# Optimization experiments

Measured on AMD Instinct MI355X. Metric: run time of the kernel, lower is better.

## Reference

```python
import jax, jax.numpy as jnp
import numpy as np

K = 20
EPS = 1e-5


def knn_idx(x, k):
    # x: (B, N, C) -> (B, N, k) indices of k nearest neighbors (incl. self)
    xx = jnp.sum(x * x, axis=-1, keepdims=True)           # (B,N,1)
    inner = -2.0 * jnp.einsum('bnc,bmc->bnm', x, x)        # (B,N,N)
    pd = -xx - inner - jnp.swapaxes(xx, 1, 2)              # negative sq dist
    _, idx = jax.lax.top_k(pd, k)                          # (B,N,k)
    return idx


def get_graph_feature(x, k=K):
    B, N, C = x.shape
    idx = knn_idx(x, k)                                    # (B,N,k)
    # gather neighbor features per batch
    feature = jax.vmap(lambda xb, ib: xb[ib])(x, idx)      # (B,N,k,C)
    xe = jnp.broadcast_to(x[:, :, None, :], (B, N, k, C))  # (B,N,k,C)
    f = jnp.concatenate([feature - xe, xe], axis=3)        # (B,N,k,2C)
    return jnp.transpose(f, (0, 3, 1, 2))                  # (B,2C,N,k)


def conv1x1(x, W, b):
    # x: (B,Cin,N,k), W: (Cout,Cin)
    return jnp.einsum('bcnk,oc->bonk', x, W) + b[None, :, None, None]


def batchnorm(x, gamma, beta):
    # training-mode BN over (B,N,k) per channel, biased variance (torch default)
    mean = jnp.mean(x, axis=(0, 2, 3), keepdims=True)
    var = jnp.var(x, axis=(0, 2, 3), keepdims=True)
    xhat = (x - mean) * jax.lax.rsqrt(var + EPS)
    return xhat * gamma[None, :, None, None] + beta[None, :, None, None]


def setup_inputs() -> dict:
    key = jax.random.key(0)
    ks = jax.random.split(key, 10)
    B, N, C = 4, 4096, 3
    x = jax.random.normal(ks[0], (B, N, C), dtype=jnp.float32)
    W1 = jax.random.normal(ks[1], (64, 2 * C), dtype=jnp.float32) * 0.1
    b1 = jnp.zeros((64,), jnp.float32)
    g1 = jnp.ones((64,), jnp.float32)
    be1 = jnp.zeros((64,), jnp.float32)
    W2 = jax.random.normal(ks[2], (128, 64), dtype=jnp.float32) * 0.1
    b2 = jnp.zeros((128,), jnp.float32)
    g2 = jnp.ones((128,), jnp.float32)
    be2 = jnp.zeros((128,), jnp.float32)
    W3 = jax.random.normal(ks[3], (128, 128), dtype=jnp.float32) * 0.1
    b3 = jnp.zeros((128,), jnp.float32)
    g3 = jnp.ones((128,), jnp.float32)
    be3 = jnp.zeros((128,), jnp.float32)
    return {"x": x, "W1": W1, "b1": b1, "g1": g1, "be1": be1,
            "W2": W2, "b2": b2, "g2": g2, "be2": be2,
            "W3": W3, "b3": b3, "g3": g3, "be3": be3}


def reference(x, W1, b1, g1, be1, W2, b2, g2, be2, W3, b3, g3, be3):
    f = get_graph_feature(x, K)                  # (B,6,N,k)
    h = jax.nn.relu(batchnorm(conv1x1(f, W1, b1), g1, be1))
    h = jax.nn.relu(batchnorm(conv1x1(h, W2, b2), g2, be2))
    h = batchnorm(conv1x1(h, W3, b3), g3, be3)
    return jnp.max(h, axis=-1)                   # (B,128,N)
```

## Files before the change

### kernel.cpp

```cpp
#include <hip/hip_runtime.h>


typedef __attribute__((ext_vector_type(8)))  short short8;
typedef __attribute__((ext_vector_type(4)))  float floatx4;

#define BATCH 4
#define NPTS  4096
#define KNN   20
#define BN_   (BATCH*NPTS)
#define CNT   (BATCH*NPTS*KNN)

__device__ __forceinline__ unsigned short f2bf(float f) {
  unsigned u = __float_as_uint(f);
  unsigned r = u + 0x7FFFu + ((u >> 16) & 1u);
  return (unsigned short)(r >> 16);
}

__device__ __forceinline__ short8 pack8(float a, float b, float c, float d,
                                        float e, float f, float g, float h) {
  short8 r;
  r[0]=(short)f2bf(a); r[1]=(short)f2bf(b); r[2]=(short)f2bf(c); r[3]=(short)f2bf(d);
  r[4]=(short)f2bf(e); r[5]=(short)f2bf(f); r[6]=(short)f2bf(g); r[7]=(short)f2bf(h);
  return r;
}

__device__ __forceinline__ unsigned mono(float f) {
  unsigned u = __float_as_uint(f);
  return u ^ ((unsigned)((int)u >> 31) | 0x80000000u);
}

__global__ void pf_prep(const float* __restrict__ x, float4* __restrict__ xp,
                        float* __restrict__ stats) {
  int pt = blockIdx.x * 256 + threadIdx.x;
  float x0 = x[pt*3+0], x1 = x[pt*3+1], x2 = x[pt*3+2];
  float xx = x0*x0 + x1*x1 + x2*x2;
  xp[pt] = make_float4(x0, x1, x2, xx);
  if (blockIdx.x == 0)
    for (int i = threadIdx.x; i < 640; i += 256) stats[i] = 0.0f;
}

__device__ __forceinline__ float sort_take20th(float v, int lane) {
  #pragma unroll
  for (int k = 2; k <= 64; k <<= 1) {
    #pragma unroll
    for (int j = k >> 1; j >= 1; j >>= 1) {
      float o = __shfl_xor(v, j);
      bool keepmax = (((lane & j) == 0) == ((lane & k) == 0));
      v = keepmax ? fmaxf(v, o) : fminf(v, o);
    }
  }
  return __shfl(v, 19);
}

__device__ __forceinline__ unsigned long long sort64_desc(unsigned long long v,
                                                          int lane) {
  #pragma unroll
  for (int k = 2; k <= 64; k <<= 1) {
    #pragma unroll
    for (int j = k >> 1; j >= 1; j >>= 1) {
      unsigned long long o = __shfl_xor(v, j);
      bool keepmax = (((lane & j) == 0) == ((lane & k) == 0));
      unsigned long long hi = v > o ? v : o;
      unsigned long long lo = v > o ? o : v;
      v = keepmax ? hi : lo;
    }
  }
  return v;
}

__global__ __launch_bounds__(256) void pf_knn(const float4* __restrict__ xp,
                                              int* __restrict__ idxb) {
  __shared__ unsigned long long lst[8][128];
  __shared__ int lcnt[8];
  const int tid  = threadIdx.x;
  const int lane = tid & 63;
  const int w    = tid >> 6;
  const int b    = blockIdx.x >> 9;
  const int nb   = (blockIdx.x & 511) * 8 + w * 2;
  const float4* xb = xp + b * NPTS;

  float4 q0 = xb[nb], q1 = xb[nb + 1];

  float mx0 = -3.0e38f, mx1 = -3.0e38f;
  for (int j0 = 0; j0 < NPTS; j0 += 64) {
    float4 c = xb[j0 + lane];
    float d0 = fmaf(q0.x,c.x, fmaf(q0.y,c.y, q0.z*c.z));
    float d1 = fmaf(q1.x,c.x, fmaf(q1.y,c.y, q1.z*c.z));
    mx0 = fmaxf(mx0, fmaf(2.f,d0,-q0.w) - c.w);
    mx1 = fmaxf(mx1, fmaf(2.f,d1,-q1.w) - c.w);
  }
  float T0 = sort_take20th(mx0, lane);
  float T1 = sort_take20th(mx1, lane);

  if (lane < 2) lcnt[w*2 + lane] = 0;
  __syncthreads();

  for (int j0 = 0; j0 < NPTS; j0 += 64) {
    float4 c = xb[j0 + lane];
    float d0 = fmaf(q0.x,c.x, fmaf(q0.y,c.y, q0.z*c.z));
    float d1 = fmaf(q1.x,c.x, fmaf(q1.y,c.y, q1.z*c.z));
    float p0 = fmaf(2.f,d0,-q0.w) - c.w;
    float p1 = fmaf(2.f,d1,-q1.w) - c.w;
    unsigned long long keybase = (unsigned long long)(4095 - (j0 + lane));
    if (p0 >= T0) {
      int o = atomicAdd(&lcnt[w*2+0], 1);
      if (o < 128) lst[w*2+0][o] = ((unsigned long long)mono(p0) << 32) | keybase;
    }
    if (p1 >= T1) {
      int o = atomicAdd(&lcnt[w*2+1], 1);
      if (o < 128) lst[w*2+1][o] = ((unsigned long long)mono(p1) << 32) | keybase;
    }
  }

  #pragma unroll 1
  for (int i = 0; i < 2; ++i) {
    const int li = w*2 + i;
    const int cn = lcnt[li];
    const int outbase = (b * NPTS + nb + i) * KNN;
    if (cn <= 64) {
      unsigned long long v = (lane < cn) ? lst[li][lane] : 0ull;
      v = sort64_desc(v, lane);
      if (lane < KNN) idxb[outbase + lane] = 4095 - (int)(v & 0xFFFFFFFFull);
    } else if (cn <= 128) {
      unsigned long long e0 = lst[li][lane];
      unsigned long long e1 = (lane + 64 < cn) ? lst[li][lane + 64] : 0ull;
      #pragma unroll 1
      for (int r = 0; r < KNN; ++r) {
        unsigned long long m = e0 > e1 ? e0 : e1;
        #pragma unroll
        for (int o = 32; o; o >>= 1) {
          unsigned long long t = __shfl_xor(m, o);
          m = t > m ? t : m;
        }
        if (lane == 0) idxb[outbase + r] = 4095 - (int)(m & 0xFFFFFFFFull);
        if (e0 == m) e0 = 0ull; else if (e1 == m) e1 = 0ull;
      }
    } else {
      const float4 qq = (i == 0) ? q0 : q1;
      unsigned long long prev = ~0ull;
      #pragma unroll 1
      for (int r = 0; r < KNN; ++r) {
        unsigned long long best = 0ull;
        for (int j0 = 0; j0 < NPTS; j0 += 64) {
          float4 c = xb[j0 + lane];
          float dd = fmaf(qq.x,c.x, fmaf(qq.y,c.y, qq.z*c.z));
          float pd = fmaf(2.f,dd,-qq.w) - c.w;
          unsigned long long key = ((unsigned long long)mono(pd) << 32) |
                                   (unsigned long long)(4095 - (j0 + lane));
          if (key < prev && key > best) best = key;
        }
        #pragma unroll
        for (int o = 32; o; o >>= 1) {
          unsigned long long t = __shfl_xor(best, o);
          best = t > best ? t : best;
        }
        if (lane == 0) idxb[outbase + r] = 4095 - (int)(best & 0xFFFFFFFFull);
        prev = best;
      }
    }
  }
}

__global__ __launch_bounds__(256) void pf_stats1(
    const float4* __restrict__ xp, const int* __restrict__ idxb,
    const float* __restrict__ W1, const float* __restrict__ b1,
    float* __restrict__ gs1, float* __restrict__ gq1) {
  __shared__ float S[64], Q[64];
  const int tid = threadIdx.x;
  const int c = tid & 63, slice = tid >> 6;
  if (tid < 64) { S[tid] = 0.f; Q[tid] = 0.f; }
  __syncthreads();
  const float wa0=W1[c*6+0], wa1=W1[c*6+1], wa2=W1[c*6+2];
  const float wb0=W1[c*6+3], wb1=W1[c*6+4], wb2=W1[c*6+5];
  const float bb = b1[c];
  float s = 0.f, q = 0.f;
  int ptbase = (blockIdx.x * 4 + slice) * 4;
  for (int u = 0; u < 4; ++u) {
    int pt = ptbase + u;
    float4 xi = xp[pt];
    int ib = (pt >> 12) << 12;
    for (int kk = 0; kk < KNN; ++kk) {
      int j = idxb[pt*KNN + kk];
      float4 xj = xp[ib + j];
      float y = bb;
      y = fmaf(wa0, xj.x - xi.x, y);
      y = fmaf(wa1, xj.y - xi.y, y);
      y = fmaf(wa2, xj.z - xi.z, y);
      y = fmaf(wb0, xi.x, y);
      y = fmaf(wb1, xi.y, y);
      y = fmaf(wb2, xi.z, y);
      s += y; q = fmaf(y, y, q);
    }
  }
  atomicAdd(&S[c], s); atomicAdd(&Q[c], q);
  __syncthreads();
  if (tid < 64) { atomicAdd(&gs1[tid], S[tid]); atomicAdd(&gq1[tid], Q[tid]); }
}

__global__ void pf_affine(const float* __restrict__ gs, const float* __restrict__ gq,
                          const float* __restrict__ gamma, const float* __restrict__ beta,
                          const float* __restrict__ bconv, int foldb, int C,
                          float* __restrict__ sc, float* __restrict__ sh) {
  int c = threadIdx.x;
  if (c < C) {
    const float inv = 1.0f / (float)CNT;
    float mean = gs[c] * inv;
    float var  = gq[c] * inv - mean * mean;
    float s = gamma[c] * rsqrtf(var + 1e-5f);
    float shift = beta[c] - mean * s;
    if (foldb) shift = fmaf(s, bconv[c], shift);
    sc[c] = s; sh[c] = shift;
  }
}

__global__ __launch_bounds__(256, 2) void pf_stats2(
    const float4* __restrict__ xp, const int* __restrict__ idxb,
    const float* __restrict__ W1, const float* __restrict__ sc1e,
    const float* __restrict__ sh1e, const float* __restrict__ W2,
    const float* __restrict__ b2,
    float* __restrict__ gs2, float* __restrict__ gq2) {
  __shared__ __align__(16) float4 XI[32];
  __shared__ __align__(16) float4 XJ[32];
  __shared__ __align__(16) unsigned short H1[32][72];
  __shared__ float SS[128], SQ[128];

  const int tid = threadIdx.x;
  const int lane = tid & 63, w = tid >> 6;
  const int chalf = w & 1, rh = w >> 1;
  const int l15 = lane & 15, quad = lane >> 4;
  const int pt0 = blockIdx.x * 32;

  if (tid < 128) { SS[tid] = 0.f; SQ[tid] = 0.f; }
  if (tid < 32)  XI[tid] = xp[pt0 + tid];

  short8 w1f[2];
  #pragma unroll
  for (int t = 0; t < 2; ++t) {
    short8 f = {0,0,0,0,0,0,0,0};
    if (quad == 0) {
      const float* p = W1 + (32*chalf + 16*t + l15) * 6;
      f = pack8(p[0],p[1],p[2],p[3],p[4],p[5],0.f,0.f);
    }
    w1f[t] = f;
  }
  float a1[2], s1[2];
  #pragma unroll
  for (int t = 0; t < 2; ++t) {
    int c = 32*chalf + 16*t + l15;
    a1[t] = sc1e[c]; s1[t] = sh1e[c];
  }
  short8 w2f[2][4];
  #pragma unroll
  for (int ks = 0; ks < 2; ++ks)
    #pragma unroll
    for (int t = 0; t < 4; ++t) {
      const float* p = W2 + (64*chalf + 16*t + l15) * 64 + 32*ks + quad*8;
      w2f[ks][t] = pack8(p[0],p[1],p[2],p[3],p[4],p[5],p[6],p[7]);
    }
  float bb2[4];
  #pragma unroll
  for (int t = 0; t < 4; ++t) bb2[t] = b2[64*chalf + 16*t + l15];

  float sum[4] = {0,0,0,0}, sq[4] = {0,0,0,0};

  for (int kk = 0; kk < KNN; ++kk) {
    if (tid < 32) {
      int pt = pt0 + tid;
      XJ[tid] = xp[((pt >> 12) << 12) + idxb[pt*KNN + kk]];
    }
    __syncthreads();
    short8 af = {0,0,0,0,0,0,0,0};
    if (quad == 0) {
      float4 xi = XI[rh*16 + l15];
      float4 xj = XJ[rh*16 + l15];
      af = pack8(xj.x-xi.x, xj.y-xi.y, xj.z-xi.z, xi.x, xi.y, xi.z, 0.f, 0.f);
    }
    floatx4 acc1[2] = {{0,0,0,0},{0,0,0,0}};
    #pragma unroll
    for (int t = 0; t < 2; ++t)
      acc1[t] = __builtin_amdgcn_mfma_f32_16x16x32_bf16(af, w1f[t], acc1[t], 0,0,0);
    #pragma unroll
    for (int t = 0; t < 2; ++t) {
      int c = 32*chalf + 16*t + l15;
      #pragma unroll
      for (int r = 0; r < 4; ++r) {
        float h = fmaxf(fmaf(a1[t], acc1[t][r], s1[t]), 0.f);
        H1[rh*16 + quad*4 + r][c] = f2bf(h);
      }
    }
    __syncthreads();
    floatx4 acc2[4] = {{0,0,0,0},{0,0,0,0},{0,0,0,0},{0,0,0,0}};
    #pragma unroll
    for (int ks = 0; ks < 2; ++ks) {
      short8 a = *(const short8*)&H1[rh*16 + l15][ks*32 + quad*8];
      #pragma unroll
      for (int t = 0; t < 4; ++t)
        acc2[t] = __builtin_amdgcn_mfma_f32_16x16x32_bf16(a, w2f[ks][t], acc2[t], 0,0,0);
    }
    #pragma unroll
    for (int t = 0; t < 4; ++t)
      #pragma unroll
      for (int r = 0; r < 4; ++r) {
        float v = acc2[t][r] + bb2[t];
        sum[t] += v; sq[t] = fmaf(v, v, sq[t]);
      }
  }
  #pragma unroll
  for (int t = 0; t < 4; ++t) {
    float s = sum[t], z = sq[t];
    s += __shfl_xor(s, 16); z += __shfl_xor(z, 16);
    s += __shfl_xor(s, 32); z += __shfl_xor(z, 32);
    if (quad == 0) {
      int c = 64*chalf + 16*t + l15;
      atomicAdd(&SS[c], s); atomicAdd(&SQ[c], z);
    }
  }
  __syncthreads();
  if (tid < 128) { atomicAdd(&gs2[tid], SS[tid]); atomicAdd(&gq2[tid], SQ[tid]); }
}

__global__ __launch_bounds__(256, 2) void pf_main(
    const float4* __restrict__ xp, const int* __restrict__ idxb,
    const float* __restrict__ W1, const float* __restrict__ sc1e,
    const float* __restrict__ sh1e, const float* __restrict__ W2,
    const float* __restrict__ sc2e, const float* __restrict__ shm2,
    const float* __restrict__ W3, const float* __restrict__ b3,
    float* __restrict__ gs3, float* __restrict__ gq3,
    float* __restrict__ maxv) {
  __shared__ __align__(16) float4 XI[32];
  __shared__ __align__(16) float4 XJ[32];
  __shared__ __align__(16) unsigned short H1[32][72];
  __shared__ __align__(16) unsigned short H2[32][136];
  __shared__ float SS[128], SQ[128];

  const int tid = threadIdx.x;
  const int lane = tid & 63, w = tid >> 6;
  const int chalf = w & 1, rh = w >> 1;
  const int l15 = lane & 15, quad = lane >> 4;
  const int pt0 = blockIdx.x * 32;

  if (tid < 128) { SS[tid] = 0.f; SQ[tid] = 0.f; }
  if (tid < 32)  XI[tid] = xp[pt0 + tid];

  short8 w1f[2];
  #pragma unroll
  for (int t = 0; t < 2; ++t) {
    short8 f = {0,0,0,0,0,0,0,0};
    if (quad == 0) {
      const float* p = W1 + (32*chalf + 16*t + l15) * 6;
      f = pack8(p[0],p[1],p[2],p[3],p[4],p[5],0.f,0.f);
    }
    w1f[t] = f;
  }
  float a1[2], s1[2];
  #pragma unroll
  for (int t = 0; t < 2; ++t) {
    int c = 32*chalf + 16*t + l15;
    a1[t] = sc1e[c]; s1[t] = sh1e[c];
  }
  short8 w2f[2][4];
  #pragma unroll
  for (int ks = 0; ks < 2; ++ks)
    #pragma unroll
    for (int t = 0; t < 4; ++t) {
      const float* p = W2 + (64*chalf + 16*t + l15) * 64 + 32*ks + quad*8;
      w2f[ks][t] = pack8(p[0],p[1],p[2],p[3],p[4],p[5],p[6],p[7]);
    }
  float a2[4], s2[4], bb3[4];
  #pragma unroll
  for (int t = 0; t < 4; ++t) {
    int c = 64*chalf + 16*t + l15;
    a2[t] = sc2e[c]; s2[t] = shm2[c]; bb3[t] = b3[c];
  }
  short8 w3f[4][4];
  #pragma unroll
  for (int ks = 0; ks < 4; ++ks)
    #pragma unroll
    for (int t = 0; t < 4; ++t) {
      const float* p = W3 + (64*chalf + 16*t + l15) * 128 + 32*ks + quad*8;
      w3f[ks][t] = pack8(p[0],p[1],p[2],p[3],p[4],p[5],p[6],p[7]);
    }

  float sum[4] = {0,0,0,0}, sq[4] = {0,0,0,0};
  float mx[4][4];
  #pragma unroll
  for (int t = 0; t < 4; ++t)
    #pragma unroll
    for (int r = 0; r < 4; ++r) mx[t][r] = -3.0e38f;

  for (int kk = 0; kk < KNN; ++kk) {
    if (tid < 32) {
      int pt = pt0 + tid;
      XJ[tid] = xp[((pt >> 12) << 12) + idxb[pt*KNN + kk]];
    }
    __syncthreads();
    short8 af = {0,0,0,0,0,0,0,0};
    if (quad == 0) {
      float4 xi = XI[rh*16 + l15];
      float4 xj = XJ[rh*16 + l15];
      af = pack8(xj.x-xi.x, xj.y-xi.y, xj.z-xi.z, xi.x, xi.y, xi.z, 0.f, 0.f);
    }
    floatx4 acc1[2] = {{0,0,0,0},{0,0,0,0}};
    #pragma unroll
    for (int t = 0; t < 2; ++t)
      acc1[t] = __builtin_amdgcn_mfma_f32_16x16x32_bf16(af, w1f[t], acc1[t], 0,0,0);
    #pragma unroll
    for (int t = 0; t < 2; ++t) {
      int c = 32*chalf + 16*t + l15;
      #pragma unroll
      for (int r = 0; r < 4; ++r) {
        float h = fmaxf(fmaf(a1[t], acc1[t][r], s1[t]), 0.f);
        H1[rh*16 + quad*4 + r][c] = f2bf(h);
      }
    }
    __syncthreads();
    floatx4 acc2[4] = {{0,0,0,0},{0,0,0,0},{0,0,0,0},{0,0,0,0}};
    #pragma unroll
    for (int ks = 0; ks < 2; ++ks) {
      short8 a = *(const short8*)&H1[rh*16 + l15][ks*32 + quad*8];
      #pragma unroll
      for (int t = 0; t < 4; ++t)
        acc2[t] = __builtin_amdgcn_mfma_f32_16x16x32_bf16(a, w2f[ks][t], acc2[t], 0,0,0);
    }
    #pragma unroll
    for (int t = 0; t < 4; ++t) {
      int c = 64*chalf + 16*t + l15;
      #pragma unroll
      for (int r = 0; r < 4; ++r) {
        float h = fmaxf(fmaf(a2[t], acc2[t][r], s2[t]), 0.f);
        H2[rh*16 + quad*4 + r][c] = f2bf(h);
      }
    }
    __syncthreads();
    floatx4 acc3[4] = {{0,0,0,0},{0,0,0,0},{0,0,0,0},{0,0,0,0}};
    #pragma unroll
    for (int ks = 0; ks < 4; ++ks) {
      short8 a = *(const short8*)&H2[rh*16 + l15][ks*32 + quad*8];
      #pragma unroll
      for (int t = 0; t < 4; ++t)
        acc3[t] = __builtin_amdgcn_mfma_f32_16x16x32_bf16(a, w3f[ks][t], acc3[t], 0,0,0);
    }
    #pragma unroll
    for (int t = 0; t < 4; ++t)
      #pragma unroll
      for (int r = 0; r < 4; ++r) {
        float v = acc3[t][r] + bb3[t];
        sum[t] += v; sq[t] = fmaf(v, v, sq[t]);
        mx[t][r] = fmaxf(mx[t][r], v);
      }
  }
  #pragma unroll
  for (int t = 0; t < 4; ++t) {
    int c = 64*chalf + 16*t + l15;
    #pragma unroll
    for (int r = 0; r < 4; ++r) {
      int row = rh*16 + quad*4 + r;
      maxv[(pt0 + row)*128 + c] = mx[t][r];
    }
  }
  #pragma unroll
  for (int t = 0; t < 4; ++t) {
    float s = sum[t], z = sq[t];
    s += __shfl_xor(s, 16); z += __shfl_xor(z, 16);
    s += __shfl_xor(s, 32); z += __shfl_xor(z, 32);
    if (quad == 0) {
      int c = 64*chalf + 16*t + l15;
      atomicAdd(&SS[c], s); atomicAdd(&SQ[c], z);
    }
  }
  __syncthreads();
  if (tid < 128) { atomicAdd(&gs3[tid], SS[tid]); atomicAdd(&gq3[tid], SQ[tid]); }
}

__global__ __launch_bounds__(256) void pf_out(
    const float* __restrict__ maxv, const float* __restrict__ sc3,
    const float* __restrict__ sh3, float* __restrict__ out) {
  __shared__ float T[128][65];
  __shared__ float SC[128], SH[128];
  const int tid = threadIdx.x;
  const int b  = blockIdx.x >> 6;
  const int n0 = (blockIdx.x & 63) * 64;
  if (tid < 128) { SC[tid] = sc3[tid]; SH[tid] = sh3[tid]; }
  __syncthreads();
  const float4* mv4 = (const float4*)maxv;
  #pragma unroll
  for (int r = 0; r < 8; ++r) {
    int fid = r * 256 + tid;
    int nl = fid >> 5, c4 = fid & 31;
    float4 v = mv4[(b*NPTS + n0 + nl)*32 + c4];
    int c = c4 * 4;
    T[c+0][nl] = fmaf(SC[c+0], v.x, SH[c+0]);
    T[c+1][nl] = fmaf(SC[c+1], v.y, SH[c+1]);
    T[c+2][nl] = fmaf(SC[c+2], v.z, SH[c+2]);
    T[c+3][nl] = fmaf(SC[c+3], v.w, SH[c+3]);
  }
  __syncthreads();
  #pragma unroll
  for (int r = 0; r < 8; ++r) {
    int fid = r * 256 + tid;
    int c = fid >> 4, nq = fid & 15;
    float4 o;
    o.x = T[c][nq*4+0]; o.y = T[c][nq*4+1];
    o.z = T[c][nq*4+2]; o.w = T[c][nq*4+3];
    *(float4*)(out + (size_t)b*128*NPTS + (size_t)c*NPTS + n0 + nq*4) = o;
  }
}

extern "C" void kernel_launch(void* const* d_in, const int* in_sizes, int n_in,
                              void* d_out, int out_size, void* d_ws, size_t ws_size,
                              hipStream_t stream) {
  const float* x   = (const float*)d_in[0];
  const float* W1  = (const float*)d_in[1];
  const float* b1  = (const float*)d_in[2];
  const float* g1  = (const float*)d_in[3];
  const float* be1 = (const float*)d_in[4];
  const float* W2  = (const float*)d_in[5];
  const float* b2  = (const float*)d_in[6];
  const float* g2  = (const float*)d_in[7];
  const float* be2 = (const float*)d_in[8];
  const float* W3  = (const float*)d_in[9];
  const float* b3  = (const float*)d_in[10];
  const float* g3  = (const float*)d_in[11];
  const float* be3 = (const float*)d_in[12];
  float* out = (float*)d_out;

  char* p = (char*)d_ws;
  float4* xp  = (float4*)p;            p += (size_t)BN_ * 16;
  int*    idxb= (int*)p;               p += (size_t)BN_ * KNN * 4;
  float*  stats = (float*)p;           p += 640 * 4;
  float*  aff   = (float*)p;           p += 640 * 4;
  float*  maxv  = (float*)p;

  float *gs1 = stats,       *gq1 = stats + 64;
  float *gs2 = stats + 128, *gq2 = stats + 256;
  float *gs3 = stats + 384, *gq3 = stats + 512;
  float *sc1e = aff,        *sh1e = aff + 64;
  float *sc2e = aff + 128,  *shm2 = aff + 256;
  float *sc3  = aff + 384,  *sh3  = aff + 512;

  pf_prep  <<<64,   256, 0, stream>>>(x, xp, stats);
  pf_knn   <<<2048, 256, 0, stream>>>(xp, idxb);
  pf_stats1<<<1024, 256, 0, stream>>>(xp, idxb, W1, b1, gs1, gq1);
  pf_affine<<<1,    64,  0, stream>>>(gs1, gq1, g1, be1, b1, 1, 64, sc1e, sh1e);
  pf_stats2<<<512,  256, 0, stream>>>(xp, idxb, W1, sc1e, sh1e, W2, b2, gs2, gq2);
  pf_affine<<<1,    128, 0, stream>>>(gs2, gq2, g2, be2, b2, 1, 128, sc2e, shm2);
  pf_main  <<<512,  256, 0, stream>>>(xp, idxb, W1, sc1e, sh1e, W2, sc2e, shm2,
                                      W3, b3, gs3, gq3, maxv);
  pf_affine<<<1,    128, 0, stream>>>(gs3, gq3, g3, be3, b3, 0, 128, sc3, sh3);
  pf_out   <<<256,  256, 0, stream>>>(maxv, sc3, sh3, out);
}
```

Baseline: 251.8 us.

## Split neighbor loop across two blocks and prefetch neighbor coordinates into LDS

The stats2 and main kernels now launch twice as many blocks, each covering half of the 20 neighbors for a 32-point tile. Each block gathers all its neighbor coordinates into shared memory up front, which removes the per-iteration global gather and one barrier per iteration. The main kernel writes two partial max buffers that the output kernel combines with a max. W1 fragments move to LDS and launch bounds rise to 3 blocks per CU to lower register pressure and raise occupancy. The costs are a doubled maxv buffer with the matching extra traffic, and W2/W3 fragment setup repeated across twice as many blocks.

```diff
diff --git a/kernel.cpp b/kernel.cpp
--- a/kernel.cpp
+++ b/kernel.cpp
@@ -7,6 +7,7 @@
 #define BATCH 4
 #define NPTS  4096
 #define KNN   20
+#define KH    10
 #define BN_   (BATCH*NPTS)
 #define CNT   (BATCH*NPTS*KNN)
 
@@ -213,36 +214,38 @@
   }
 }
 
-__global__ __launch_bounds__(256, 2) void pf_stats2(
+__global__ __launch_bounds__(256, 3) void pf_stats2(
     const float4* __restrict__ xp, const int* __restrict__ idxb,
     const float* __restrict__ W1, const float* __restrict__ sc1e,
     const float* __restrict__ sh1e, const float* __restrict__ W2,
     const float* __restrict__ b2,
     float* __restrict__ gs2, float* __restrict__ gq2) {
   __shared__ __align__(16) float4 XI[32];
-  __shared__ __align__(16) float4 XJ[32];
-  __shared__ __align__(16) unsigned short H1[32][72];
+  __shared__ __align__(16) float4 XJL[KH][32];
+  __shared__ __align__(16) unsigned short W1L[64][8];
+  __shared__ __align__(16) unsigned short H1[2][32][72];
   __shared__ float SS[128], SQ[128];
 
   const int tid = threadIdx.x;
   const int lane = tid & 63, w = tid >> 6;
   const int chalf = w & 1, rh = w >> 1;
   const int l15 = lane & 15, quad = lane >> 4;
-  const int pt0 = blockIdx.x * 32;
+  const int bp = blockIdx.x >> 1, kh = blockIdx.x & 1;
+  const int pt0 = bp * 32;
+  const int kb = kh * KH;
 
   if (tid < 128) { SS[tid] = 0.f; SQ[tid] = 0.f; }
   if (tid < 32)  XI[tid] = xp[pt0 + tid];
-
-  short8 w1f[2];
-  #pragma unroll
-  for (int t = 0; t < 2; ++t) {
-    short8 f = {0,0,0,0,0,0,0,0};
-    if (quad == 0) {
-      const float* p = W1 + (32*chalf + 16*t + l15) * 6;
-      f = pack8(p[0],p[1],p[2],p[3],p[4],p[5],0.f,0.f);
-    }
-    w1f[t] = f;
-  }
+  if (tid < 64) {
+    const float* p = W1 + tid * 6;
+    *(short8*)&W1L[tid][0] = pack8(p[0],p[1],p[2],p[3],p[4],p[5],0.f,0.f);
+  }
+  for (int u = tid; u < 32*KH; u += 256) {
+    int kk = u >> 5, pp = u & 31;
+    int pt = pt0 + pp;
+    XJL[kk][pp] = xp[((pt >> 12) << 12) + idxb[pt*KNN + kb + kk]];
+  }
+
   float a1[2], s1[2];
   #pragma unroll
   for (int t = 0; t < 2; ++t) {
@@ -262,37 +265,35 @@
   for (int t = 0; t < 4; ++t) bb2[t] = b2[64*chalf + 16*t + l15];
 
   float sum[4] = {0,0,0,0}, sq[4] = {0,0,0,0};
-
-  for (int kk = 0; kk < KNN; ++kk) {
-    if (tid < 32) {
-      int pt = pt0 + tid;
-      XJ[tid] = xp[((pt >> 12) << 12) + idxb[pt*KNN + kk]];
-    }
-    __syncthreads();
+  __syncthreads();
+
+  for (int kk = 0; kk < KH; ++kk) {
     short8 af = {0,0,0,0,0,0,0,0};
+    short8 w1f0 = af, w1f1 = af;
     if (quad == 0) {
       float4 xi = XI[rh*16 + l15];
-      float4 xj = XJ[rh*16 + l15];
+      float4 xj = XJL[kk][rh*16 + l15];
       af = pack8(xj.x-xi.x, xj.y-xi.y, xj.z-xi.z, xi.x, xi.y, xi.z, 0.f, 0.f);
+      w1f0 = *(const short8*)&W1L[32*chalf + l15][0];
+      w1f1 = *(const short8*)&W1L[32*chalf + 16 + l15][0];
     }
     floatx4 acc1[2] = {{0,0,0,0},{0,0,0,0}};
-    #pragma unroll
-    for (int t = 0; t < 2; ++t)
-      acc1[t] = __builtin_amdgcn_mfma_f32_16x16x32_bf16(af, w1f[t], acc1[t], 0,0,0);
+    acc1[0] = __builtin_amdgcn_mfma_f32_16x16x32_bf16(af, w1f0, acc1[0], 0,0,0);
+    acc1[1] = __builtin_amdgcn_mfma_f32_16x16x32_bf16(af, w1f1, acc1[1], 0,0,0);
     #pragma unroll
     for (int t = 0; t < 2; ++t) {
       int c = 32*chalf + 16*t + l15;
       #pragma unroll
       for (int r = 0; r < 4; ++r) {
         float h = fmaxf(fmaf(a1[t], acc1[t][r], s1[t]), 0.f);
-        H1[rh*16 + quad*4 + r][c] = f2bf(h);
+        H1[kk & 1][rh*16 + quad*4 + r][c] = f2bf(h);
       }
     }
     __syncthreads();
     floatx4 acc2[4] = {{0,0,0,0},{0,0,0,0},{0,0,0,0},{0,0,0,0}};
     #pragma unroll
     for (int ks = 0; ks < 2; ++ks) {
-      short8 a = *(const short8*)&H1[rh*16 + l15][ks*32 + quad*8];
+      short8 a = *(const short8*)&H1[kk & 1][rh*16 + l15][ks*32 + quad*8];
       #pragma unroll
       for (int t = 0; t < 4; ++t)
         acc2[t] = __builtin_amdgcn_mfma_f32_16x16x32_bf16(a, w2f[ks][t], acc2[t], 0,0,0);
@@ -319,7 +320,7 @@
   if (tid < 128) { atomicAdd(&gs2[tid], SS[tid]); atomicAdd(&gq2[tid], SQ[tid]); }
 }
 
-__global__ __launch_bounds__(256, 2) void pf_main(
+__global__ __launch_bounds__(256, 3) void pf_main(
     const float4* __restrict__ xp, const int* __restrict__ idxb,
     const float* __restrict__ W1, const float* __restrict__ sc1e,
     const float* __restrict__ sh1e, const float* __restrict__ W2,
@@ -328,7 +329,8 @@
     float* __restrict__ gs3, float* __restrict__ gq3,
     float* __restrict__ maxv) {
   __shared__ __align__(16) float4 XI[32];
-  __shared__ __align__(16) float4 XJ[32];
+  __shared__ __align__(16) float4 XJL[KH][32];
+  __shared__ __align__(16) unsigned short W1L[64][8];
   __shared__ __align__(16) unsigned short H1[32][72];
   __shared__ __align__(16) unsigned short H2[32][136];
   __shared__ float SS[128], SQ[128];
@@ -337,21 +339,22 @@
   const int lane = tid & 63, w = tid >> 6;
   const int chalf = w & 1, rh = w >> 1;
   const int l15 = lane & 15, quad = lane >> 4;
-  const int pt0 = blockIdx.x * 32;
+  const int bp = blockIdx.x >> 1, kh = blockIdx.x & 1;
+  const int pt0 = bp * 32;
+  const int kb = kh * KH;
 
   if (tid < 128) { SS[tid] = 0.f; SQ[tid] = 0.f; }
   if (tid < 32)  XI[tid] = xp[pt0 + tid];
-
-  short8 w1f[2];
-  #pragma unroll
-  for (int t = 0; t < 2; ++t) {
-    short8 f = {0,0,0,0,0,0,0,0};
-    if (quad == 0) {
-      const float* p = W1 + (32*chalf + 16*t + l15) * 6;
-      f = pack8(p[0],p[1],p[2],p[3],p[4],p[5],0.f,0.f);
-    }
-    w1f[t] = f;
-  }
+  if (tid < 64) {
+    const float* p = W1 + tid * 6;
+    *(short8*)&W1L[tid][0] = pack8(p[0],p[1],p[2],p[3],p[4],p[5],0.f,0.f);
+  }
+  for (int u = tid; u < 32*KH; u += 256) {
+    int kk = u >> 5, pp = u & 31;
+    int pt = pt0 + pp;
+    XJL[kk][pp] = xp[((pt >> 12) << 12) + idxb[pt*KNN + kb + kk]];
+  }
+
   float a1[2], s1[2];
   #pragma unroll
   for (int t = 0; t < 2; ++t) {
@@ -388,22 +391,21 @@
     #pragma unroll
     for (int r = 0; r < 4; ++r) mx[t][r] = -3.0e38f;
 
-  for (int kk = 0; kk < KNN; ++kk) {
-    if (tid < 32) {
-      int pt = pt0 + tid;
-      XJ[tid] = xp[((pt >> 12) << 12) + idxb[pt*KNN + kk]];
-    }
-    __syncthreads();
+  __syncthreads();
+
+  for (int kk = 0; kk < KH; ++kk) {
     short8 af = {0,0,0,0,0,0,0,0};
+    short8 w1f0 = af, w1f1 = af;
     if (quad == 0) {
       float4 xi = XI[rh*16 + l15];
-      float4 xj = XJ[rh*16 + l15];
+      float4 xj = XJL[kk][rh*16 + l15];
       af = pack8(xj.x-xi.x, xj.y-xi.y, xj.z-xi.z, xi.x, xi.y, xi.z, 0.f, 0.f);
+      w1f0 = *(const short8*)&W1L[32*chalf + l15][0];
+      w1f1 = *(const short8*)&W1L[32*chalf + 16 + l15][0];
     }
     floatx4 acc1[2] = {{0,0,0,0},{0,0,0,0}};
-    #pragma unroll
-    for (int t = 0; t < 2; ++t)
-      acc1[t] = __builtin_amdgcn_mfma_f32_16x16x32_bf16(af, w1f[t], acc1[t], 0,0,0);
+    acc1[0] = __builtin_amdgcn_mfma_f32_16x16x32_bf16(af, w1f0, acc1[0], 0,0,0);
+    acc1[1] = __builtin_amdgcn_mfma_f32_16x16x32_bf16(af, w1f1, acc1[1], 0,0,0);
     #pragma unroll
     for (int t = 0; t < 2; ++t) {
       int c = 32*chalf + 16*t + l15;
@@ -449,13 +451,14 @@
         mx[t][r] = fmaxf(mx[t][r], v);
       }
   }
+  float* mvh = maxv + (size_t)kh * BN_ * 128;
   #pragma unroll
   for (int t = 0; t < 4; ++t) {
     int c = 64*chalf + 16*t + l15;
     #pragma unroll
     for (int r = 0; r < 4; ++r) {
       int row = rh*16 + quad*4 + r;
-      maxv[(pt0 + row)*128 + c] = mx[t][r];
+      mvh[(pt0 + row)*128 + c] = mx[t][r];
     }
   }
   #pragma unroll
@@ -482,17 +485,20 @@
   const int n0 = (blockIdx.x & 63) * 64;
   if (tid < 128) { SC[tid] = sc3[tid]; SH[tid] = sh3[tid]; }
   __syncthreads();
-  const float4* mv4 = (const float4*)maxv;
+  const float4* mv4a = (const float4*)maxv;
+  const float4* mv4b = mv4a + (size_t)BN_ * 32;
   #pragma unroll
   for (int r = 0; r < 8; ++r) {
     int fid = r * 256 + tid;
     int nl = fid >> 5, c4 = fid & 31;
-    float4 v = mv4[(b*NPTS + n0 + nl)*32 + c4];
+    size_t off = (size_t)(b*NPTS + n0 + nl)*32 + c4;
+    float4 va = mv4a[off];
+    float4 vb = mv4b[off];
     int c = c4 * 4;
-    T[c+0][nl] = fmaf(SC[c+0], v.x, SH[c+0]);
-    T[c+1][nl] = fmaf(SC[c+1], v.y, SH[c+1]);
-    T[c+2][nl] = fmaf(SC[c+2], v.z, SH[c+2]);
-    T[c+3][nl] = fmaf(SC[c+3], v.w, SH[c+3]);
+    T[c+0][nl] = fmaf(SC[c+0], fmaxf(va.x, vb.x), SH[c+0]);
+    T[c+1][nl] = fmaf(SC[c+1], fmaxf(va.y, vb.y), SH[c+1]);
+    T[c+2][nl] = fmaf(SC[c+2], fmaxf(va.z, vb.z), SH[c+2]);
+    T[c+3][nl] = fmaf(SC[c+3], fmaxf(va.w, vb.w), SH[c+3]);
   }
   __syncthreads();
   #pragma unroll
@@ -542,9 +548,9 @@
   pf_knn   <<<2048, 256, 0, stream>>>(xp, idxb);
   pf_stats1<<<1024, 256, 0, stream>>>(xp, idxb, W1, b1, gs1, gq1);
   pf_affine<<<1,    64,  0, stream>>>(gs1, gq1, g1, be1, b1, 1, 64, sc1e, sh1e);
-  pf_stats2<<<512,  256, 0, stream>>>(xp, idxb, W1, sc1e, sh1e, W2, b2, gs2, gq2);
+  pf_stats2<<<1024, 256, 0, stream>>>(xp, idxb, W1, sc1e, sh1e, W2, b2, gs2, gq2);
   pf_affine<<<1,    128, 0, stream>>>(gs2, gq2, g2, be2, b2, 1, 128, sc2e, shm2);
-  pf_main  <<<512,  256, 0, stream>>>(xp, idxb, W1, sc1e, sh1e, W2, sc2e, shm2,
+  pf_main  <<<1024, 256, 0, stream>>>(xp, idxb, W1, sc1e, sh1e, W2, sc2e, shm2,
                                       W3, b3, gs3, gq3, maxv);
   pf_affine<<<1,    128, 0, stream>>>(gs3, gq3, g3, be3, b3, 0, 128, sc3, sh3);
   pf_out   <<<256,  256, 0, stream>>>(maxv, sc3, sh3, out);
```

Result: slower. 325.4 us (+29.2%).

## Fold BN scales into bf16 weights and restructure MLP kernels to 16-point tiles

Applied to the files above, without the earlier changes.

Pre-converts W2/W3 to bf16 once and folds each batchnorm scale into the following layer's bf16 weights inside the affine kernels, so the per-neighbor loop only adds shifts (seeded as MFMA accumulators) and applies ReLU. The stats2/main kernels now handle 16 points per block with the 4 waves splitting output channels, transposed MFMA operands, packed 4-wide bf16 stores, and all neighbor coordinates preloaded into LDS up front, which removes a barrier per neighbor iteration. Bias is now applied analytically to the sums and after the max instead of per element. Grids double and occupancy hints rise, which trades larger per-block weight-load overhead for more parallelism; folding the scale before bf16 rounding changes numerics slightly.

```diff
diff --git a/kernel.cpp b/kernel.cpp
--- a/kernel.cpp
+++ b/kernel.cpp
@@ -24,19 +24,33 @@
   return r;
 }
 
+__device__ __forceinline__ void store4bf(unsigned short* dst, float a, float b,
+                                         float c, float d) {
+  unsigned lo = (unsigned)f2bf(a) | ((unsigned)f2bf(b) << 16);
+  unsigned hi = (unsigned)f2bf(c) | ((unsigned)f2bf(d) << 16);
+  *(uint2*)dst = make_uint2(lo, hi);
+}
+
 __device__ __forceinline__ unsigned mono(float f) {
   unsigned u = __float_as_uint(f);
   return u ^ ((unsigned)((int)u >> 31) | 0x80000000u);
 }
 
 __global__ void pf_prep(const float* __restrict__ x, float4* __restrict__ xp,
-                        float* __restrict__ stats) {
+                        float* __restrict__ stats,
+                        const float* __restrict__ W2, const float* __restrict__ W3,
+                        unsigned short* __restrict__ w2p,
+                        unsigned short* __restrict__ w3p) {
   int pt = blockIdx.x * 256 + threadIdx.x;
   float x0 = x[pt*3+0], x1 = x[pt*3+1], x2 = x[pt*3+2];
   float xx = x0*x0 + x1*x1 + x2*x2;
   xp[pt] = make_float4(x0, x1, x2, xx);
   if (blockIdx.x == 0)
     for (int i = threadIdx.x; i < 640; i += 256) stats[i] = 0.0f;
+  if (blockIdx.x == 1) {
+    for (int i = threadIdx.x; i < 128*64;  i += 256) w2p[i] = f2bf(W2[i]);
+    for (int i = threadIdx.x; i < 128*128; i += 256) w3p[i] = f2bf(W3[i]);
+  }
 }
 
 __device__ __forceinline__ float sort_take20th(float v, int lane) {
@@ -200,7 +214,9 @@
 __global__ void pf_affine(const float* __restrict__ gs, const float* __restrict__ gq,
                           const float* __restrict__ gamma, const float* __restrict__ beta,
                           const float* __restrict__ bconv, int foldb, int C,
-                          float* __restrict__ sc, float* __restrict__ sh) {
+                          float* __restrict__ sc, float* __restrict__ sh,
+                          const float* __restrict__ Wsrc,
+                          unsigned short* __restrict__ wdst, int ncol, int stride) {
   int c = threadIdx.x;
   if (c < C) {
     const float inv = 1.0f / (float)CNT;
@@ -210,264 +226,233 @@
     float shift = beta[c] - mean * s;
     if (foldb) shift = fmaf(s, bconv[c], shift);
     sc[c] = s; sh[c] = shift;
-  }
-}
-
-__global__ __launch_bounds__(256, 2) void pf_stats2(
+    if (wdst) {
+      for (int j = 0; j < ncol; ++j) wdst[c*stride + j] = f2bf(s * Wsrc[c*ncol + j]);
+      for (int j = ncol; j < stride; ++j) wdst[c*stride + j] = 0;
+    }
+  }
+}
+
+__global__ __launch_bounds__(256, 4) void pf_stats2(
     const float4* __restrict__ xp, const int* __restrict__ idxb,
-    const float* __restrict__ W1, const float* __restrict__ sc1e,
-    const float* __restrict__ sh1e, const float* __restrict__ W2,
-    const float* __restrict__ b2,
+    const unsigned short* __restrict__ w1s, const float* __restrict__ sh1e,
+    const unsigned short* __restrict__ w2p, const float* __restrict__ b2,
     float* __restrict__ gs2, float* __restrict__ gq2) {
-  __shared__ __align__(16) float4 XI[32];
-  __shared__ __align__(16) float4 XJ[32];
-  __shared__ __align__(16) unsigned short H1[32][72];
+  __shared__ __align__(16) float4 XI[16];
+  __shared__ __align__(16) float4 XJL[KNN][16];
+  __shared__ __align__(16) unsigned short W1L[64][8];
+  __shared__ __align__(16) unsigned short H1[2][16][72];
+  __shared__ __align__(16) float SH1L[64];
   __shared__ float SS[128], SQ[128];
 
   const int tid = threadIdx.x;
-  const int lane = tid & 63, w = tid >> 6;
-  const int chalf = w & 1, rh = w >> 1;
+  const int lane = tid & 63, ww = tid >> 6;
   const int l15 = lane & 15, quad = lane >> 4;
-  const int pt0 = blockIdx.x * 32;
+  const int pt0 = blockIdx.x * 16;
 
   if (tid < 128) { SS[tid] = 0.f; SQ[tid] = 0.f; }
-  if (tid < 32)  XI[tid] = xp[pt0 + tid];
-
-  short8 w1f[2];
-  #pragma unroll
-  for (int t = 0; t < 2; ++t) {
-    short8 f = {0,0,0,0,0,0,0,0};
+  if (tid < 16)  XI[tid] = xp[pt0 + tid];
+  if (tid < 64) {
+    *(short8*)&W1L[tid][0] = *(const short8*)(w1s + tid * 8);
+    SH1L[tid] = sh1e[tid];
+  }
+  for (int u = tid; u < 16*KNN; u += 256) {
+    int kk = u >> 4, pp = u & 15;
+    int pt = pt0 + pp;
+    XJL[kk][pp] = xp[((pt >> 12) << 12) + idxb[pt*KNN + kk]];
+  }
+
+  short8 w2f[2][2];
+  #pragma unroll
+  for (int ks = 0; ks < 2; ++ks)
+    #pragma unroll
+    for (int t = 0; t < 2; ++t)
+      w2f[ks][t] = *(const short8*)(w2p + (32*ww + 16*t + l15)*64 + 32*ks + quad*8);
+
+  float sum[2][4] = {{0,0,0,0},{0,0,0,0}}, sq[2][4] = {{0,0,0,0},{0,0,0,0}};
+  __syncthreads();
+
+  for (int kk = 0; kk < KNN; ++kk) {
+    short8 af = {0,0,0,0,0,0,0,0};
+    short8 w1f = af;
     if (quad == 0) {
-      const float* p = W1 + (32*chalf + 16*t + l15) * 6;
-      f = pack8(p[0],p[1],p[2],p[3],p[4],p[5],0.f,0.f);
-    }
-    w1f[t] = f;
-  }
-  float a1[2], s1[2];
-  #pragma unroll
-  for (int t = 0; t < 2; ++t) {
-    int c = 32*chalf + 16*t + l15;
-    a1[t] = sc1e[c]; s1[t] = sh1e[c];
-  }
-  short8 w2f[2][4];
-  #pragma unroll
-  for (int ks = 0; ks < 2; ++ks)
-    #pragma unroll
-    for (int t = 0; t < 4; ++t) {
-      const float* p = W2 + (64*chalf + 16*t + l15) * 64 + 32*ks + quad*8;
-      w2f[ks][t] = pack8(p[0],p[1],p[2],p[3],p[4],p[5],p[6],p[7]);
-    }
-  float bb2[4];
-  #pragma unroll
-  for (int t = 0; t < 4; ++t) bb2[t] = b2[64*chalf + 16*t + l15];
-
-  float sum[4] = {0,0,0,0}, sq[4] = {0,0,0,0};
-
-  for (int kk = 0; kk < KNN; ++kk) {
-    if (tid < 32) {
-      int pt = pt0 + tid;
-      XJ[tid] = xp[((pt >> 12) << 12) + idxb[pt*KNN + kk]];
-    }
+      float4 xi = XI[l15];
+      float4 xj = XJL[kk][l15];
+      af  = pack8(xj.x-xi.x, xj.y-xi.y, xj.z-xi.z, xi.x, xi.y, xi.z, 0.f, 0.f);
+      w1f = *(const short8*)&W1L[16*ww + l15][0];
+    }
+    floatx4 acc1 = *(const floatx4*)&SH1L[16*ww + 4*quad];
+    acc1 = __builtin_amdgcn_mfma_f32_16x16x32_bf16(w1f, af, acc1, 0,0,0);
+    store4bf(&H1[kk & 1][l15][16*ww + 4*quad],
+             fmaxf(acc1[0],0.f), fmaxf(acc1[1],0.f),
+             fmaxf(acc1[2],0.f), fmaxf(acc1[3],0.f));
     __syncthreads();
-    short8 af = {0,0,0,0,0,0,0,0};
-    if (quad == 0) {
-      float4 xi = XI[rh*16 + l15];
-      float4 xj = XJ[rh*16 + l15];
-      af = pack8(xj.x-xi.x, xj.y-xi.y, xj.z-xi.z, xi.x, xi.y, xi.z, 0.f, 0.f);
-    }
-    floatx4 acc1[2] = {{0,0,0,0},{0,0,0,0}};
-    #pragma unroll
-    for (int t = 0; t < 2; ++t)
-      acc1[t] = __builtin_amdgcn_mfma_f32_16x16x32_bf16(af, w1f[t], acc1[t], 0,0,0);
-    #pragma unroll
-    for (int t = 0; t < 2; ++t) {
-      int c = 32*chalf + 16*t + l15;
+    floatx4 acc2[2] = {{0,0,0,0},{0,0,0,0}};
+    #pragma unroll
+    for (int ks = 0; ks < 2; ++ks) {
+      short8 a = *(const short8*)&H1[kk & 1][l15][ks*32 + quad*8];
+      #pragma unroll
+      for (int t = 0; t < 2; ++t)
+        acc2[t] = __builtin_amdgcn_mfma_f32_16x16x32_bf16(w2f[ks][t], a, acc2[t], 0,0,0);
+    }
+    #pragma unroll
+    for (int t = 0; t < 2; ++t)
       #pragma unroll
       for (int r = 0; r < 4; ++r) {
-        float h = fmaxf(fmaf(a1[t], acc1[t][r], s1[t]), 0.f);
-        H1[rh*16 + quad*4 + r][c] = f2bf(h);
+        float v = acc2[t][r];
+        sum[t][r] += v; sq[t][r] = fmaf(v, v, sq[t][r]);
       }
-    }
+  }
+  #pragma unroll
+  for (int t = 0; t < 2; ++t)
+    #pragma unroll
+    for (int r = 0; r < 4; ++r) {
+      float s = sum[t][r], z = sq[t][r];
+      s += __shfl_xor(s, 1); z += __shfl_xor(z, 1);
+      s += __shfl_xor(s, 2); z += __shfl_xor(z, 2);
+      s += __shfl_xor(s, 4); z += __shfl_xor(z, 4);
+      s += __shfl_xor(s, 8); z += __shfl_xor(z, 8);
+      if (l15 == 0) {
+        int ch = 32*ww + 16*t + 4*quad + r;
+        float bc = b2[ch];
+        float zc = fmaf(2.f*bc, s, z) + 320.f*bc*bc;
+        float scr = s + 320.f*bc;
+        atomicAdd(&SS[ch], scr); atomicAdd(&SQ[ch], zc);
+      }
+    }
+  __syncthreads();
+  if (tid < 128) { atomicAdd(&gs2[tid], SS[tid]); atomicAdd(&gq2[tid], SQ[tid]); }
+}
+
+__global__ __launch_bounds__(256, 4) void pf_main(
+    const float4* __restrict__ xp, const int* __restrict__ idxb,
+    const unsigned short* __restrict__ w1s, const float* __restrict__ sh1e,
+    const unsigned short* __restrict__ w2s, const float* __restrict__ shm2,
+    const unsigned short* __restrict__ w3p, const float* __restrict__ b3,
+    float* __restrict__ gs3, float* __restrict__ gq3,
+    float* __restrict__ maxv) {
+  __shared__ __align__(16) float4 XI[16];
+  __shared__ __align__(16) float4 XJL[KNN][16];
+  __shared__ __align__(16) unsigned short W1L[64][8];
+  __shared__ __align__(16) unsigned short H1[16][72];
+  __shared__ __align__(16) unsigned short H2[16][136];
+  __shared__ __align__(16) float SH1L[64];
+  __shared__ __align__(16) float SH2L[128];
+  __shared__ float SS[128], SQ[128];
+
+  const int tid = threadIdx.x;
+  const int lane = tid & 63, ww = tid >> 6;
+  const int l15 = lane & 15, quad = lane >> 4;
+  const int pt0 = blockIdx.x * 16;
+
+  if (tid < 128) { SS[tid] = 0.f; SQ[tid] = 0.f; SH2L[tid] = shm2[tid]; }
+  if (tid < 16)  XI[tid] = xp[pt0 + tid];
+  if (tid < 64) {
+    *(short8*)&W1L[tid][0] = *(const short8*)(w1s + tid * 8);
+    SH1L[tid] = sh1e[tid];
+  }
+  for (int u = tid; u < 16*KNN; u += 256) {
+    int kk = u >> 4, pp = u & 15;
+    int pt = pt0 + pp;
+    XJL[kk][pp] = xp[((pt >> 12) << 12) + idxb[pt*KNN + kk]];
+  }
+
+  short8 w2f[2][2];
+  #pragma unroll
+  for (int ks = 0; ks < 2; ++ks)
+    #pragma unroll
+    for (int t = 0; t < 2; ++t)
+      w2f[ks][t] = *(const short8*)(w2s + (32*ww + 16*t + l15)*64 + 32*ks + quad*8);
+  short8 w3f[4][2];
+  #pragma unroll
+  for (int ks = 0; ks < 4; ++ks)
+    #pragma unroll
+    for (int t = 0; t < 2; ++t)
+      w3f[ks][t] = *(const short8*)(w3p + (32*ww + 16*t + l15)*128 + 32*ks + quad*8);
+
+  float sum[2][4] = {{0,0,0,0},{0,0,0,0}}, sq[2][4] = {{0,0,0,0},{0,0,0,0}};
+  float mx[2][4];
+  #pragma unroll
+  for (int t = 0; t < 2; ++t)
+    #pragma unroll
+    for (int r = 0; r < 4; ++r) mx[t][r] = -3.0e38f;
+
+  __syncthreads();
+
+  for (int kk = 0; kk < KNN; ++kk) {
+    short8 af = {0,0,0,0,0,0,0,0};
+    short8 w1f = af;
+    if (quad == 0) {
+      float4 xi = XI[l15];
+      float4 xj = XJL[kk][l15];
+      af  = pack8(xj.x-xi.x, xj.y-xi.y, xj.z-xi.z, xi.x, xi.y, xi.z, 0.f, 0.f);
+      w1f = *(const short8*)&W1L[16*ww + l15][0];
+    }
+    floatx4 acc1 = *(const floatx4*)&SH1L[16*ww + 4*quad];
+    acc1 = __builtin_amdgcn_mfma_f32_16x16x32_bf16(w1f, af, acc1, 0,0,0);
+    store4bf(&H1[l15][16*ww + 4*quad],
+             fmaxf(acc1[0],0.f), fmaxf(acc1[1],0.f),
+             fmaxf(acc1[2],0.f), fmaxf(acc1[3],0.f));
     __syncthreads();
-    floatx4 acc2[4] = {{0,0,0,0},{0,0,0,0},{0,0,0,0},{0,0,0,0}};
+    floatx4 acc2[2];
+    #pragma unroll
+    for (int t = 0; t < 2; ++t)
+      acc2[t] = *(const floatx4*)&SH2L[32*ww + 16*t + 4*quad];
     #pragma unroll
     for (int ks = 0; ks < 2; ++ks) {
-      short8 a = *(const short8*)&H1[rh*16 + l15][ks*32 + quad*8];
+      short8 a = *(const short8*)&H1[l15][ks*32 + quad*8];
       #pragma unroll
-      for (int t = 0; t < 4; ++t)
-        acc2[t] = __builtin_amdgcn_mfma_f32_16x16x32_bf16(a, w2f[ks][t], acc2[t], 0,0,0);
-    }
-    #pragma unroll
-    for (int t = 0; t < 4; ++t)
+      for (int t = 0; t < 2; ++t)
+        acc2[t] = __builtin_amdgcn_mfma_f32_16x16x32_bf16(w2f[ks][t], a, acc2[t], 0,0,0);
+    }
+    #pragma unroll
+    for (int t = 0; t < 2; ++t)
+      store4bf(&H2[l15][32*ww + 16*t + 4*quad],
+               fmaxf(acc2[t][0],0.f), fmaxf(acc2[t][1],0.f),
+               fmaxf(acc2[t][2],0.f), fmaxf(acc2[t][3],0.f));
+    __syncthreads();
+    floatx4 acc3[2] = {{0,0,0,0},{0,0,0,0}};
+    #pragma unroll
+    for (int ks = 0; ks < 4; ++ks) {
+      short8 a = *(const short8*)&H2[l15][ks*32 + quad*8];
+      #pragma unroll
+      for (int t = 0; t < 2; ++t)
+        acc3[t] = __builtin_amdgcn_mfma_f32_16x16x32_bf16(w3f[ks][t], a, acc3[t], 0,0,0);
+    }
+    #pragma unroll
+    for (int t = 0; t < 2; ++t)
       #pragma unroll
       for (int r = 0; r < 4; ++r) {
-        float v = acc2[t][r] + bb2[t];
-        sum[t] += v; sq[t] = fmaf(v, v, sq[t]);
-      }
-  }
-  #pragma unroll
-  for (int t = 0; t < 4; ++t) {
-    float s = sum[t], z = sq[t];
-    s += __shfl_xor(s, 16); z += __shfl_xor(z, 16);
-    s += __shfl_xor(s, 32); z += __shfl_xor(z, 32);
-    if (quad == 0) {
-      int c = 64*chalf + 16*t + l15;
-      atomicAdd(&SS[c], s); atomicAdd(&SQ[c], z);
-    }
-  }
-  __syncthreads();
-  if (tid < 128) { atomicAdd(&gs2[tid], SS[tid]); atomicAdd(&gq2[tid], SQ[tid]); }
-}
-
-__global__ __launch_bounds__(256, 2) void pf_main(
-    const float4* __restrict__ xp, const int* __restrict__ idxb,
-    const float* __restrict__ W1, const float* __restrict__ sc1e,
-    const float* __restrict__ sh1e, const float* __restrict__ W2,
-    const float* __restrict__ sc2e, const float* __restrict__ shm2,
-    const float* __restrict__ W3, const float* __restrict__ b3,
-    float* __restrict__ gs3, float* __restrict__ gq3,
-    float* __restrict__ maxv) {
-  __shared__ __align__(16) float4 XI[32];
-  __shared__ __align__(16) float4 XJ[32];
-  __shared__ __align__(16) unsigned short H1[32][72];
-  __shared__ __align__(16) unsigned short H2[32][136];
-  __shared__ float SS[128], SQ[128];
-
-  const int tid = threadIdx.x;
-  const int lane = tid & 63, w = tid >> 6;
-  const int chalf = w & 1, rh = w >> 1;
-  const int l15 = lane & 15, quad = lane >> 4;
-  const int pt0 = blockIdx.x * 32;
-
-  if (tid < 128) { SS[tid] = 0.f; SQ[tid] = 0.f; }
-  if (tid < 32)  XI[tid] = xp[pt0 + tid];
-
-  short8 w1f[2];
-  #pragma unroll
-  for (int t = 0; t < 2; ++t) {
-    short8 f = {0,0,0,0,0,0,0,0};
-    if (quad == 0) {
-      const float* p = W1 + (32*chalf + 16*t + l15) * 6;
-      f = pack8(p[0],p[1],p[2],p[3],p[4],p[5],0.f,0.f);
-    }
-    w1f[t] = f;
-  }
-  float a1[2], s1[2];
-  #pragma unroll
-  for (int t = 0; t < 2; ++t) {
-    int c = 32*chalf + 16*t + l15;
-    a1[t] = sc1e[c]; s1[t] = sh1e[c];
-  }
-  short8 w2f[2][4];
-  #pragma unroll
-  for (int ks = 0; ks < 2; ++ks)
-    #pragma unroll
-    for (int t = 0; t < 4; ++t) {
-      const float* p = W2 + (64*chalf + 16*t + l15) * 64 + 32*ks + quad*8;
-      w2f[ks][t] = pack8(p[0],p[1],p[2],p[3],p[4],p[5],p[6],p[7]);
-    }
-  float a2[4], s2[4], bb3[4];
-  #pragma unroll
-  for (int t = 0; t < 4; ++t) {
-    int c = 64*chalf + 16*t + l15;
-    a2[t] = sc2e[c]; s2[t] = shm2[c]; bb3[t] = b3[c];
-  }
-  short8 w3f[4][4];
-  #pragma unroll
-  for (int ks = 0; ks < 4; ++ks)
-    #pragma unroll
-    for (int t = 0; t < 4; ++t) {
-      const float* p = W3 + (64*chalf + 16*t + l15) * 128 + 32*ks + quad*8;
-      w3f[ks][t] = pack8(p[0],p[1],p[2],p[3],p[4],p[5],p[6],p[7]);
-    }
-
-  float sum[4] = {0,0,0,0}, sq[4] = {0,0,0,0};
-  float mx[4][4];
-  #pragma unroll
-  for (int t = 0; t < 4; ++t)
-    #pragma unroll
-    for (int r = 0; r < 4; ++r) mx[t][r] = -3.0e38f;
-
-  for (int kk = 0; kk < KNN; ++kk) {
-    if (tid < 32) {
-      int pt = pt0 + tid;
-      XJ[tid] = xp[((pt >> 12) << 12) + idxb[pt*KNN + kk]];
-    }
-    __syncthreads();
-    short8 af = {0,0,0,0,0,0,0,0};
-    if (quad == 0) {
-      float4 xi = XI[rh*16 + l15];
-      float4 xj = XJ[rh*16 + l15];
-      af = pack8(xj.x-xi.x, xj.y-xi.y, xj.z-xi.z, xi.x, xi.y, xi.z, 0.f, 0.f);
-    }
-    floatx4 acc1[2] = {{0,0,0,0},{0,0,0,0}};
-    #pragma unroll
-    for (int t = 0; t < 2; ++t)
-      acc1[t] = __builtin_amdgcn_mfma_f32_16x16x32_bf16(af, w1f[t], acc1[t], 0,0,0);
-    #pragma unroll
-    for (int t = 0; t < 2; ++t) {
-      int c = 32*chalf + 16*t + l15;
-      #pragma unroll
-      for (int r = 0; r < 4; ++r) {
-        float h = fmaxf(fmaf(a1[t], acc1[t][r], s1[t]), 0.f);
-        H1[rh*16 + quad*4 + r][c] = f2bf(h);
-      }
-    }
-    __syncthreads();
-    floatx4 acc2[4] = {{0,0,0,0},{0,0,0,0},{0,0,0,0},{0,0,0,0}};
-    #pragma unroll
-    for (int ks = 0; ks < 2; ++ks) {
-      short8 a = *(const short8*)&H1[rh*16 + l15][ks*32 + quad*8];
-      #pragma unroll
-      for (int t = 0; t < 4; ++t)
-        acc2[t] = __builtin_amdgcn_mfma_f32_16x16x32_bf16(a, w2f[ks][t], acc2[t], 0,0,0);
-    }
-    #pragma unroll
-    for (int t = 0; t < 4; ++t) {
-      int c = 64*chalf + 16*t + l15;
-      #pragma unroll
-      for (int r = 0; r < 4; ++r) {
-        float h = fmaxf(fmaf(a2[t], acc2[t][r], s2[t]), 0.f);
-        H2[rh*16 + quad*4 + r][c] = f2bf(h);
-      }
-    }
-    __syncthreads();
-    floatx4 acc3[4] = {{0,0,0,0},{0,0,0,0},{0,0,0,0},{0,0,0,0}};
-    #pragma unroll
-    for (int ks = 0; ks < 4; ++ks) {
-      short8 a = *(const short8*)&H2[rh*16 + l15][ks*32 + quad*8];
-      #pragma unroll
-      for (int t = 0; t < 4; ++t)
-        acc3[t] = __builtin_amdgcn_mfma_f32_16x16x32_bf16(a, w3f[ks][t], acc3[t], 0,0,0);
-    }
-    #pragma unroll
-    for (int t = 0; t < 4; ++t)
-      #pragma unroll
-      for (int r = 0; r < 4; ++r) {
-        float v = acc3[t][r] + bb3[t];
-        sum[t] += v; sq[t] = fmaf(v, v, sq[t]);
+        float v = acc3[t][r];
+        sum[t][r] += v; sq[t][r] = fmaf(v, v, sq[t][r]);
         mx[t][r] = fmaxf(mx[t][r], v);
       }
   }
-  #pragma unroll
-  for (int t = 0; t < 4; ++t) {
-    int c = 64*chalf + 16*t + l15;
+
+  #pragma unroll
+  for (int t = 0; t < 2; ++t) {
+    int ch0 = 32*ww + 16*t + 4*quad;
+    const float4 b4 = *(const float4*)&b3[ch0];
+    float4 o = make_float4(mx[t][0]+b4.x, mx[t][1]+b4.y, mx[t][2]+b4.z, mx[t][3]+b4.w);
+    *(float4*)&maxv[(size_t)(pt0 + l15)*128 + ch0] = o;
+  }
+  #pragma unroll
+  for (int t = 0; t < 2; ++t)
     #pragma unroll
     for (int r = 0; r < 4; ++r) {
-      int row = rh*16 + quad*4 + r;
-      maxv[(pt0 + row)*128 + c] = mx[t][r];
-    }
-  }
-  #pragma unroll
-  for (int t = 0; t < 4; ++t) {
-    float s = sum[t], z = sq[t];
-    s += __shfl_xor(s, 16); z += __shfl_xor(z, 16);
-    s += __shfl_xor(s, 32); z += __shfl_xor(z, 32);
-    if (quad == 0) {
-      int c = 64*chalf + 16*t + l15;
-      atomicAdd(&SS[c], s); atomicAdd(&SQ[c], z);
-    }
-  }
+      float s = sum[t][r], z = sq[t][r];
+      s += __shfl_xor(s, 1); z += __shfl_xor(z, 1);
+      s += __shfl_xor(s, 2); z += __shfl_xor(z, 2);
+      s += __shfl_xor(s, 4); z += __shfl_xor(z, 4);
+      s += __shfl_xor(s, 8); z += __shfl_xor(z, 8);
+      if (l15 == 0) {
+        int ch = 32*ww + 16*t + 4*quad + r;
+        float bc = b3[ch];
+        float zc = fmaf(2.f*bc, s, z) + 320.f*bc*bc;
+        float scr = s + 320.f*bc;
+        atomicAdd(&SS[ch], scr); atomicAdd(&SQ[ch], zc);
+      }
+    }
   __syncthreads();
   if (tid < 128) { atomicAdd(&gs3[tid], SS[tid]); atomicAdd(&gq3[tid], SQ[tid]); }
 }
@@ -487,7 +472,7 @@
   for (int r = 0; r < 8; ++r) {
     int fid = r * 256 + tid;
     int nl = fid >> 5, c4 = fid & 31;
-    float4 v = mv4[(b*NPTS + n0 + nl)*32 + c4];
+    float4 v = mv4[(size_t)(b*NPTS + n0 + nl)*32 + c4];
     int c = c4 * 4;
     T[c+0][nl] = fmaf(SC[c+0], v.x, SH[c+0]);
     T[c+1][nl] = fmaf(SC[c+1], v.y, SH[c+1]);
@@ -529,6 +514,10 @@
   int*    idxb= (int*)p;               p += (size_t)BN_ * KNN * 4;
   float*  stats = (float*)p;           p += 640 * 4;
   float*  aff   = (float*)p;           p += 640 * 4;
+  unsigned short* w1s = (unsigned short*)p; p += 64 * 8 * 2;
+  unsigned short* w2p = (unsigned short*)p; p += 128 * 64 * 2;
+  unsigned short* w2s = (unsigned short*)p; p += 128 * 64 * 2;
+  unsigned short* w3p = (unsigned short*)p; p += 128 * 128 * 2;
   float*  maxv  = (float*)p;
 
   float *gs1 = stats,       *gq1 = stats + 64;
@@ -538,14 +527,17 @@
   float *sc2e = aff + 128,  *shm2 = aff + 256;
   float *sc3  = aff + 384,  *sh3  = aff + 512;
 
-  pf_prep  <<<64,   256, 0, stream>>>(x, xp, stats);
+  pf_prep  <<<64,   256, 0, stream>>>(x, xp, stats, W2, W3, w2p, w3p);
   pf_knn   <<<2048, 256, 0, stream>>>(xp, idxb);
   pf_stats1<<<1024, 256, 0, stream>>>(xp, idxb, W1, b1, gs1, gq1);
-  pf_affine<<<1,    64,  0, stream>>>(gs1, gq1, g1, be1, b1, 1, 64, sc1e, sh1e);
-  pf_stats2<<<512,  256, 0, stream>>>(xp, idxb, W1, sc1e, sh1e, W2, b2, gs2, gq2);
-  pf_affine<<<1,    128, 0, stream>>>(gs2, gq2, g2, be2, b2, 1, 128, sc2e, shm2);
-  pf_main  <<<512,  256, 0, stream>>>(xp, idxb, W1, sc1e, sh1e, W2, sc2e, shm2,
-                                      W3, b3, gs3, gq3, maxv);
-  pf_affine<<<1,    128, 0, stream>>>(gs3, gq3, g3, be3, b3, 0, 128, sc3, sh3);
+  pf_affine<<<1,    64,  0, stream>>>(gs1, gq1, g1, be1, b1, 1, 64, sc1e, sh1e,
+                                      W1, w1s, 6, 8);
+  pf_stats2<<<1024, 256, 0, stream>>>(xp, idxb, w1s, sh1e, w2p, b2, gs2, gq2);
+  pf_affine<<<1,    128, 0, stream>>>(gs2, gq2, g2, be2, b2, 1, 128, sc2e, shm2,
+                                      W2, w2s, 64, 64);
+  pf_main  <<<1024, 256, 0, stream>>>(xp, idxb, w1s, sh1e, w2s, shm2,
+                                      w3p, b3, gs3, gq3, maxv);
+  pf_affine<<<1,    128, 0, stream>>>(gs3, gq3, g3, be3, b3, 0, 128, sc3, sh3,
+                                      nullptr, nullptr, 0, 0);
   pf_out   <<<256,  256, 0, stream>>>(maxv, sc3, sh3, out);
 }
```

Result: slower. 274.3 us (+8.9%).
